# Kernel optimization log

Hardware: AMD Instinct MI355X
Metric: run time of the kernel (lower is better)

Reference implementation:

```python
import jax, jax.numpy as jnp
import numpy as np

B, Lq, Lkv = 4, 1024, 4096
Cq, Ckv, E, NH = 512, 512, 512, 8
HD = E // NH


def setup_inputs() -> dict:
    key = jax.random.key(0)
    ks = jax.random.split(key, 8)
    s = 0.02
    return {
        "Xq": jax.random.normal(ks[0], (B, Lq, Cq), dtype=jnp.float32),
        "Xkv": jax.random.normal(ks[1], (B, Lkv, Ckv), dtype=jnp.float32),
        "mask": jax.random.randint(ks[2], (B, Lq, 1), 0, 2, dtype=jnp.int32),
        "Wq": jax.random.normal(ks[3], (Cq, E), dtype=jnp.float32) * s,
        "bq": jnp.zeros((E,), dtype=jnp.float32),
        "Wkv": jax.random.normal(ks[4], (Ckv, 2 * E), dtype=jnp.float32) * s,
        "bkv": jnp.zeros((2 * E,), dtype=jnp.float32),
        "Wp": jax.random.normal(ks[5], (E, E), dtype=jnp.float32) * s,
        "bp": jnp.zeros((E,), dtype=jnp.float32),
        "attn_pos": jax.random.normal(ks[6], (1, NH, Lq, Lkv), dtype=jnp.float32) * s,
    }


def reference(Xq, Xkv, mask, Wq, bq, Wkv, bkv, Wp, bp, attn_pos):
    scale = HD ** -0.5
    # projections
    Q = (Xq @ Wq + bq).reshape(B, Lq, NH, HD).transpose(0, 2, 1, 3) * scale  # [B,NH,Lq,HD]
    KV = (Xkv @ Wkv + bkv).reshape(B, Lkv, 2, NH, HD)
    K = KV[:, :, 0].transpose(0, 2, 1, 3)  # [B,NH,Lkv,HD]
    V = KV[:, :, 1].transpose(0, 2, 1, 3)
    # scores + learned positional bias
    attn = jnp.einsum('bhqd,bhkd->bhqk', Q, K) + attn_pos  # [B,NH,Lq,Lkv]
    # dummy-column masked softmax (mask: [B,Lq,1], 1=keep row)
    m = mask.astype(attn.dtype)[:, None]           # [B,1,Lq,1]
    attn = attn + (1.0 - m) * (-100.0)             # suppress masked query rows
    dummy = jnp.broadcast_to(jnp.where(m == 0, 100.0, -100.0), (B, NH, Lq, 1))
    attn = jax.nn.softmax(jnp.concatenate([attn, dummy], axis=-1), axis=-1)[..., :Lkv]
    # weighted sum + output projection (dropout = identity in eval)
    out = jnp.einsum('bhqk,bhkd->bhqd', attn, V)
    out = out.transpose(0, 2, 1, 3).reshape(B, Lq, E)
    return out @ Wp + bp
```

## Files before the change

### kernel.cpp

```cpp
#include <hip/hip_runtime.h>

typedef unsigned short u16;
typedef __attribute__((ext_vector_type(8))) short bf16x8;
typedef __attribute__((ext_vector_type(4))) float f32x4;
typedef __attribute__((ext_vector_type(2))) unsigned u32x2;
typedef __attribute__((ext_vector_type(4))) unsigned u32x4;

__device__ __forceinline__ u16 f2bf(float x) {
    union { float f; unsigned u; } v; v.f = x;
    unsigned r = v.u + 0x7FFF + ((v.u >> 16) & 1);
    return (u16)(r >> 16);
}

__device__ __forceinline__ unsigned cvt_pk_bf16(float lo, float hi) {
    unsigned r;
    asm("v_cvt_pk_bf16_f32 %0, %1, %2" : "=v"(r) : "v"(lo), "v"(hi));
    return r;
}

__device__ __forceinline__ bf16x8 pk8(const f32x4& s0, const f32x4& s1) {
    union { u32x4 u; bf16x8 v; } x;
    x.u[0] = cvt_pk_bf16(s0[0], s0[1]);
    x.u[1] = cvt_pk_bf16(s0[2], s0[3]);
    x.u[2] = cvt_pk_bf16(s1[0], s1[1]);
    x.u[3] = cvt_pk_bf16(s1[2], s1[3]);
    return x.v;
}

__device__ __forceinline__ void gl_lds16(const u16* g, u16* l) {
    __builtin_amdgcn_global_load_lds((const __attribute__((address_space(1))) void*)g,
                                     (__attribute__((address_space(3))) void*)l, 16, 0, 0);
}

__global__ __launch_bounds__(256) void conv_bf16_2(const float* __restrict__ Xq,
                                                   const float* __restrict__ Xkv,
                                                   u16* __restrict__ oq,
                                                   u16* __restrict__ okv) {
    int bid = blockIdx.x;
    const float* in;
    u16* out;
    size_t i;
    if (bid < 1024) {
        in = Xq; out = oq;
        i = ((size_t)bid * 256 + threadIdx.x) * 8;
    } else {
        in = Xkv; out = okv;
        i = ((size_t)(bid - 1024) * 256 + threadIdx.x) * 8;
    }
    const float4* p = (const float4*)(in + i);
    float4 a = p[0], b = p[1];
    u32x4 w = {cvt_pk_bf16(a.x, a.y), cvt_pk_bf16(a.z, a.w),
               cvt_pk_bf16(b.x, b.y), cvt_pk_bf16(b.z, b.w)};
    *(u32x4*)(out + i) = w;
}

__global__ __launch_bounds__(256) void transpose_w3(const float* __restrict__ Wq,
                                                    const float* __restrict__ Wkv,
                                                    const float* __restrict__ Wp,
                                                    u16* __restrict__ WqT,
                                                    u16* __restrict__ WkvT,
                                                    u16* __restrict__ WpT) {
    __shared__ float tile[64][65];
    int bid = blockIdx.x;
    const float* in;
    u16* out;
    int R = 512, C, bx, by;
    if (bid < 64) {
        in = Wq; out = WqT; C = 512; bx = bid & 7; by = bid >> 3;
    } else if (bid < 192) {
        bid -= 64;
        in = Wkv; out = WkvT; C = 1024; bx = bid & 15; by = bid >> 4;
    } else {
        bid -= 192;
        in = Wp; out = WpT; C = 512; bx = bid & 7; by = bid >> 3;
    }
    int r0 = by * 64, c0 = bx * 64;
    int tid = threadIdx.x;
#pragma unroll
    for (int j = 0; j < 16; ++j) {
        int e = tid + j * 256;
        int row = e >> 6, col = e & 63;
        tile[row][col] = in[(size_t)(r0 + row) * C + c0 + col];
    }
    __syncthreads();
#pragma unroll
    for (int j = 0; j < 16; ++j) {
        int e = tid + j * 256;
        int row = e >> 6, col = e & 63;
        out[(size_t)(c0 + row) * R + r0 + col] = f2bf(tile[col][row]);
    }
}

template <int MODE>
__global__ __launch_bounds__(256) void gemm_kernel(const u16* __restrict__ A,
                                                   const u16* __restrict__ Bt,
                                                   const float* __restrict__ bias,
                                                   void* __restrict__ Cout,
                                                   void* __restrict__ Cout2,
                                                   int M, int N, int K) {
    __shared__ u16 Al[128][64];
    __shared__ u16 Bl[128][64];
    int tid = threadIdx.x;
    int lane = tid & 63, wid = tid >> 6;
    int wr = wid >> 1, wc = wid & 1;
    int l15 = lane & 15, g = lane >> 4;
    int bm = blockIdx.y, bn = blockIdx.x;
    int ldr = lane >> 3, ldc = (lane & 7) << 3;

    f32x4 acc[4][4];
#pragma unroll
    for (int m = 0; m < 4; ++m)
#pragma unroll
        for (int n = 0; n < 4; ++n)
#pragma unroll
            for (int j = 0; j < 4; ++j) acc[m][n][j] = 0.f;

    int nK = K >> 6;
    for (int kt = 0; kt < nK; ++kt) {
        __syncthreads();
#pragma unroll
        for (int i = 0; i < 4; ++i) {
            int c = wid * 4 + i;
            int row = c * 8 + ldr;
            gl_lds16(A + (size_t)(bm * 128 + row) * K + kt * 64 + ldc, &Al[0][0] + c * 512);
            gl_lds16(Bt + (size_t)(bn * 128 + row) * K + kt * 64 + ldc, &Bl[0][0] + c * 512);
        }
        __syncthreads();

#pragma unroll
        for (int kk = 0; kk < 2; ++kk) {
            bf16x8 af[4], bfr[4];
#pragma unroll
            for (int m = 0; m < 4; ++m)
                af[m] = *(const bf16x8*)&Al[wr * 64 + m * 16 + l15][kk * 32 + g * 8];
#pragma unroll
            for (int n = 0; n < 4; ++n)
                bfr[n] = *(const bf16x8*)&Bl[wc * 64 + n * 16 + l15][kk * 32 + g * 8];
#pragma unroll
            for (int m = 0; m < 4; ++m)
#pragma unroll
                for (int n = 0; n < 4; ++n)
                    acc[m][n] =
                        __builtin_amdgcn_mfma_f32_16x16x32_bf16(af[m], bfr[n], acc[m][n], 0, 0, 0);
        }
    }

#pragma unroll
    for (int m = 0; m < 4; ++m)
#pragma unroll
        for (int n = 0; n < 4; ++n)
#pragma unroll
            for (int j = 0; j < 4; ++j) {
                int row = bm * 128 + wr * 64 + m * 16 + g * 4 + j;
                int col = bn * 128 + wc * 64 + n * 16 + l15;
                float v = acc[m][n][j] + bias[col];
                if (MODE == 1) {
                    int b = row >> 12, kv = row & 4095;
                    if (col < 512) {
                        int h = col >> 6, d = col & 63;
                        ((u16*)Cout)[(((size_t)((b * 8 + h) * 4096 + kv)) << 6) + d] = f2bf(v);
                    } else {
                        int c2 = col - 512;
                        int h = c2 >> 6, d = c2 & 63;
                        int p = j | ((m & 1) << 2) | (g << 3);
                        int dkv = (kv & ~31) | p;
                        ((u16*)Cout2)[((size_t)(b * 8 + h) * 64 + d) * 4096 + dkv] = f2bf(v);
                    }
                } else {
                    ((float*)Cout)[(size_t)row * N + col] = v;
                }
            }
}

template <int MODE>
__global__ __launch_bounds__(256) void gemm_n64(const u16* __restrict__ A,
                                                const u16* __restrict__ Bt,
                                                const float* __restrict__ bias,
                                                void* __restrict__ Cout,
                                                int M, int N, int K) {
    __shared__ u16 Al[128][64];
    __shared__ u16 Bl[64][64];
    int tid = threadIdx.x;
    int lane = tid & 63, wid = tid >> 6;
    int wr = wid >> 1, wc = wid & 1;
    int l15 = lane & 15, g = lane >> 4;
    int bm = blockIdx.y, bn = blockIdx.x;
    int ldr = lane >> 3, ldc = (lane & 7) << 3;

    f32x4 acc[4][2];
#pragma unroll
    for (int m = 0; m < 4; ++m)
#pragma unroll
        for (int n = 0; n < 2; ++n)
#pragma unroll
            for (int j = 0; j < 4; ++j) acc[m][n][j] = 0.f;

    int nK = K >> 6;
    for (int kt = 0; kt < nK; ++kt) {
        __syncthreads();
#pragma unroll
        for (int i = 0; i < 6; ++i) {
            int c = wid * 6 + i;
            if (c < 16) {
                int row = c * 8 + ldr;
                gl_lds16(A + (size_t)(bm * 128 + row) * K + kt * 64 + ldc, &Al[0][0] + c * 512);
            } else {
                int cb = c - 16;
                int row = cb * 8 + ldr;
                gl_lds16(Bt + (size_t)(bn * 64 + row) * K + kt * 64 + ldc, &Bl[0][0] + cb * 512);
            }
        }
        __syncthreads();

#pragma unroll
        for (int kk = 0; kk < 2; ++kk) {
            bf16x8 af[4], bfr[2];
#pragma unroll
            for (int m = 0; m < 4; ++m)
                af[m] = *(const bf16x8*)&Al[wr * 64 + m * 16 + l15][kk * 32 + g * 8];
#pragma unroll
            for (int n = 0; n < 2; ++n)
                bfr[n] = *(const bf16x8*)&Bl[wc * 32 + n * 16 + l15][kk * 32 + g * 8];
#pragma unroll
            for (int m = 0; m < 4; ++m)
#pragma unroll
                for (int n = 0; n < 2; ++n)
                    acc[m][n] =
                        __builtin_amdgcn_mfma_f32_16x16x32_bf16(af[m], bfr[n], acc[m][n], 0, 0, 0);
        }
    }

#pragma unroll
    for (int m = 0; m < 4; ++m)
#pragma unroll
        for (int n = 0; n < 2; ++n)
#pragma unroll
            for (int j = 0; j < 4; ++j) {
                int row = bm * 128 + wr * 64 + m * 16 + g * 4 + j;
                int col = bn * 64 + wc * 32 + n * 16 + l15;
                float v = acc[m][n][j] + bias[col];
                if (MODE == 0) {
                    int b = row >> 10, q = row & 1023, h = col >> 6, d = col & 63;
                    ((u16*)Cout)[(((size_t)((b * 8 + h) * 1024 + q)) << 6) + d] =
                        f2bf(v * 0.18033688011112042f);
                } else {
                    ((float*)Cout)[(size_t)row * N + col] = v;
                }
            }
}

__global__ __launch_bounds__(256, 2) void attn_kernel(const u16* __restrict__ Qb,
                                                      const u16* __restrict__ Kb,
                                                      const u16* __restrict__ Vt,
                                                      const float* __restrict__ pos,
                                                      float* __restrict__ Opart,
                                                      float* __restrict__ Lp) {
    __shared__ u16 Klds[2][4][2048];
    __shared__ u16 Vlds[2][4][2048];

    int idx = blockIdx.x;
    int h = idx & 7;
    int rest = idx >> 3;
    int qt = rest & 15, sp = rest >> 4;
    int q0 = qt * 64;
    int kvbase = sp * 1024;
    int tid = threadIdx.x, lane = tid & 63, wid = tid >> 6;
    int l15 = lane & 15, g = lane >> 4;

    bf16x8 aq[4][2];
#pragma unroll
    for (int b = 0; b < 4; ++b) {
        const u16* qp =
            Qb + (((size_t)((b * 8 + h) * 1024 + q0 + wid * 16 + l15)) << 6) + g * 8;
        aq[b][0] = *(const bf16x8*)(qp);
        aq[b][1] = *(const bf16x8*)(qp + 32);
    }

    f32x4 o[4][4];
    f32x4 lacc[4];
#pragma unroll
    for (int b = 0; b < 4; ++b) {
#pragma unroll
        for (int j = 0; j < 4; ++j) lacc[b][j] = 0.f;
#pragma unroll
        for (int n = 0; n < 4; ++n)
#pragma unroll
            for (int j = 0; j < 4; ++j) o[b][n][j] = 0.f;
    }

    const u16* Kg = Kb + ((size_t)(wid * 8 + h)) * 4096 * 64;
    const u16* Vg = Vt + ((size_t)(wid * 8 + h)) * 4096 * 64;
    int lr = lane >> 3;
    int lcs = ((lane & 7) ^ lr) << 3;
    int vhalf = (lane >> 2) & 1;
    int vslot = (lane & 3) ^ (lr & 3);

    const float* posq =
        pos + (size_t)h * 1024 * 4096 + (size_t)(q0 + wid * 16 + l15) * 4096 + kvbase;

    const short one_s = (short)0x3F80;
    bf16x8 ones = {one_s, one_s, one_s, one_s, one_s, one_s, one_s, one_s};
    int sw = (l15 & 7) << 4;

    auto STAGE = [&](int buf, int t) {
        int kv0 = kvbase + t * 32;
#pragma unroll
        for (int c = 0; c < 4; ++c) {
            gl_lds16(Kg + (size_t)(kv0 + c * 8 + lr) * 64 + lcs, &Klds[buf][wid][c * 512]);
            gl_lds16(Vg + (size_t)(2 * (c * 8 + lr) + vhalf) * 4096 + kv0 + vslot * 8,
                     &Vlds[buf][wid][c * 512]);
        }
    };

    STAGE(0, 0);
    f32x4 zr[2];
#pragma unroll
    for (int n = 0; n < 2; ++n) {
        zr[n] = *(const f32x4*)(posq + n * 16 + g * 4);
#pragma unroll
        for (int j = 0; j < 4; ++j) zr[n][j] *= 1.44269504f;
    }

    for (int kt = 0; kt < 32; ++kt) {
        int cur = kt & 1;
        __syncthreads();

        f32x4 zn0, zn1;
        if (kt < 31) {
            zn0 = *(const f32x4*)(posq + (kt + 1) * 32 + g * 4);
            zn1 = *(const f32x4*)(posq + (kt + 1) * 32 + 16 + g * 4);
            __builtin_amdgcn_sched_barrier(0);
            STAGE(cur ^ 1, kt + 1);
        }

#pragma unroll
        for (int b = 0; b < 4; ++b) {
            const char* KbL = (const char*)&Klds[cur][b][0];
            const char* VbL = (const char*)&Vlds[cur][b][0];

            f32x4 s[2];
            __builtin_amdgcn_s_setprio(1);
#pragma unroll
            for (int n = 0; n < 2; ++n) {
                bf16x8 kb0 = *(const bf16x8*)(KbL + (n * 16 + l15) * 128 + ((g * 16) ^ sw));
                bf16x8 kb1 = *(const bf16x8*)(KbL + (n * 16 + l15) * 128 + ((64 + g * 16) ^ sw));
                f32x4 t = __builtin_amdgcn_mfma_f32_16x16x32_bf16(kb0, aq[b][0], zr[n], 0, 0, 0);
                s[n] = __builtin_amdgcn_mfma_f32_16x16x32_bf16(kb1, aq[b][1], t, 0, 0, 0);
            }
            __builtin_amdgcn_s_setprio(0);

#pragma unroll
            for (int n = 0; n < 2; ++n)
#pragma unroll
                for (int j = 0; j < 4; ++j) s[n][j] = __builtin_exp2f(s[n][j]);

            bf16x8 pa = pk8(s[0], s[1]);

            __builtin_amdgcn_s_setprio(1);
#pragma unroll
            for (int n = 0; n < 4; ++n) {
                int vd = n * 16 + l15;
                int vr = vd >> 1;
                int vbyte = (vr << 7) + ((vd & 1) << 6) + (((g ^ (vr & 3)) & 3) << 4);
                bf16x8 vb = *(const bf16x8*)(VbL + vbyte);
                o[b][n] = __builtin_amdgcn_mfma_f32_16x16x32_bf16(pa, vb, o[b][n], 0, 0, 0);
            }
            lacc[b] = __builtin_amdgcn_mfma_f32_16x16x32_bf16(pa, ones, lacc[b], 0, 0, 0);
            __builtin_amdgcn_s_setprio(0);
        }

        if (kt < 31) {
#pragma unroll
            for (int j = 0; j < 4; ++j) {
                zr[0][j] = zn0[j] * 1.44269504f;
                zr[1][j] = zn1[j] * 1.44269504f;
            }
        }
    }

#pragma unroll
    for (int b = 0; b < 4; ++b) {
        int obase = (sp * 32 + b * 8 + h) * 1024;
#pragma unroll
        for (int j = 0; j < 4; ++j) {
            int row = q0 + wid * 16 + g * 4 + j;
#pragma unroll
            for (int n = 0; n < 4; ++n)
                __builtin_nontemporal_store(o[b][n][j],
                                            &Opart[((size_t)(obase + row)) * 64 + n * 16 + l15]);
            if (l15 == 0) __builtin_nontemporal_store(lacc[b][j], &Lp[obase + row]);
        }
    }
}

__global__ __launch_bounds__(256) void attn_combine(const float* __restrict__ Opart,
                                                    const float* __restrict__ Lp,
                                                    const int* __restrict__ mask,
                                                    u16* __restrict__ AO) {
    int tid = threadIdx.x;
    int d = tid & 63;
    int r = blockIdx.x * 4 + (tid >> 6);
    int bh = r >> 10, q = r & 1023;
    int b = bh >> 3, h = bh & 7;

    float L = 0.f, val = 0.f;
#pragma unroll
    for (int s2 = 0; s2 < 4; ++s2) {
        size_t rr = (size_t)(s2 * 32 + bh) * 1024 + q;
        L += Lp[rr];
        val += Opart[rr * 64 + d];
    }
    float res = mask[b * 1024 + q] ? (val / L) : 0.f;
    AO[((size_t)(b * 1024 + q)) * 512 + h * 64 + d] = f2bf(res);
}

extern "C" void kernel_launch(void* const* d_in, const int* in_sizes, int n_in,
                              void* d_out, int out_size, void* d_ws, size_t ws_size,
                              hipStream_t stream) {
    const float* Xq = (const float*)d_in[0];
    const float* Xkv = (const float*)d_in[1];
    const int* mask = (const int*)d_in[2];
    const float* Wq = (const float*)d_in[3];
    const float* bq = (const float*)d_in[4];
    const float* Wkv = (const float*)d_in[5];
    const float* bkv = (const float*)d_in[6];
    const float* Wp = (const float*)d_in[7];
    const float* bp = (const float*)d_in[8];
    const float* pos = (const float*)d_in[9];
    float* out = (float*)d_out;

    char* ws = (char*)d_ws;
    u16* WqT = (u16*)(ws);
    u16* WkvT = (u16*)(ws + 524288);
    u16* WpT = (u16*)(ws + 1572864);
    u16* Qb = (u16*)(ws + 2097152);
    u16* Kb = (u16*)(ws + 6291456);
    u16* Vt = (u16*)(ws + 23068672);
    u16* AO = (u16*)(ws + 39845888);
    float* Opart = (float*)(ws + 44040192);
    u16* Xkvb = (u16*)(ws + 44040192);
    u16* Xqb = (u16*)(ws + 60817408);
    float* Lp = (float*)(ws + 111149056);

    conv_bf16_2<<<dim3(5120), 256, 0, stream>>>(Xq, Xkv, Xqb, Xkvb);
    transpose_w3<<<dim3(256), 256, 0, stream>>>(Wq, Wkv, Wp, WqT, WkvT, WpT);
    gemm_n64<0><<<dim3(8, 32), 256, 0, stream>>>(Xqb, WqT, bq, Qb, 4096, 512, 512);
    gemm_kernel<1><<<dim3(8, 128), 256, 0, stream>>>(Xkvb, WkvT, bkv, Kb, Vt, 16384, 1024, 512);
    attn_kernel<<<dim3(512), 256, 0, stream>>>(Qb, Kb, Vt, pos, Opart, Lp);
    attn_combine<<<dim3(8192), 256, 0, stream>>>(Opart, Lp, mask, AO);
    gemm_n64<2><<<dim3(8, 32), 256, 0, stream>>>(AO, WpT, bp, out, 4096, 512, 512);
}
```

Before: 190.8 us.

## Drop LDS double buffering in attention kernel to raise occupancy to four blocks

Removes the ping-pong K/V LDS buffers and the register prefetch of the next positional-bias tile. Each iteration now loads its tile synchronously between two barriers, and launch bounds ask for four resident blocks per CU instead of two. The aim is to hide memory latency through higher occupancy rather than software pipelining, which halves LDS use and frees prefetch registers. The cost is exposed load latency inside each block, an extra barrier per iteration, and possible register spilling under the tighter launch bound.

```diff
diff --git a/kernel.cpp b/kernel.cpp
--- a/kernel.cpp
+++ b/kernel.cpp
@@ -249,14 +249,14 @@
             }
 }
 
-__global__ __launch_bounds__(256, 2) void attn_kernel(const u16* __restrict__ Qb,
+__global__ __launch_bounds__(256, 4) void attn_kernel(const u16* __restrict__ Qb,
                                                       const u16* __restrict__ Kb,
                                                       const u16* __restrict__ Vt,
                                                       const float* __restrict__ pos,
                                                       float* __restrict__ Opart,
                                                       float* __restrict__ Lp) {
-    __shared__ u16 Klds[2][4][2048];
-    __shared__ u16 Vlds[2][4][2048];
+    __shared__ u16 Klds[4][2048];
+    __shared__ u16 Vlds[4][2048];
 
     int idx = blockIdx.x;
     int h = idx & 7;
@@ -290,6 +290,8 @@
 
     const u16* Kg = Kb + ((size_t)(wid * 8 + h)) * 4096 * 64;
     const u16* Vg = Vt + ((size_t)(wid * 8 + h)) * 4096 * 64;
+    u16* KldsW = &Klds[wid][0];
+    u16* VldsW = &Vlds[wid][0];
     int lr = lane >> 3;
     int lcs = ((lane & 7) ^ lr) << 3;
     int vhalf = (lane >> 2) & 1;
@@ -302,41 +304,29 @@
     bf16x8 ones = {one_s, one_s, one_s, one_s, one_s, one_s, one_s, one_s};
     int sw = (l15 & 7) << 4;
 
-    auto STAGE = [&](int buf, int t) {
-        int kv0 = kvbase + t * 32;
-#pragma unroll
-        for (int c = 0; c < 4; ++c) {
-            gl_lds16(Kg + (size_t)(kv0 + c * 8 + lr) * 64 + lcs, &Klds[buf][wid][c * 512]);
+    f32x4 zr[2];
+    for (int kt = 0; kt < 32; ++kt) {
+        int kv0 = kvbase + kt * 32;
+        __syncthreads();
+#pragma unroll
+        for (int c = 0; c < 4; ++c)
+            gl_lds16(Kg + (size_t)(kv0 + c * 8 + lr) * 64 + lcs, KldsW + c * 512);
+#pragma unroll
+        for (int c = 0; c < 4; ++c)
             gl_lds16(Vg + (size_t)(2 * (c * 8 + lr) + vhalf) * 4096 + kv0 + vslot * 8,
-                     &Vlds[buf][wid][c * 512]);
-        }
-    };
-
-    STAGE(0, 0);
-    f32x4 zr[2];
-#pragma unroll
-    for (int n = 0; n < 2; ++n) {
-        zr[n] = *(const f32x4*)(posq + n * 16 + g * 4);
-#pragma unroll
-        for (int j = 0; j < 4; ++j) zr[n][j] *= 1.44269504f;
-    }
-
-    for (int kt = 0; kt < 32; ++kt) {
-        int cur = kt & 1;
-        __syncthreads();
-
-        f32x4 zn0, zn1;
-        if (kt < 31) {
-            zn0 = *(const f32x4*)(posq + (kt + 1) * 32 + g * 4);
-            zn1 = *(const f32x4*)(posq + (kt + 1) * 32 + 16 + g * 4);
-            __builtin_amdgcn_sched_barrier(0);
-            STAGE(cur ^ 1, kt + 1);
-        }
+                     VldsW + c * 512);
+#pragma unroll
+        for (int n = 0; n < 2; ++n) {
+            zr[n] = *(const f32x4*)(posq + kt * 32 + n * 16 + g * 4);
+#pragma unroll
+            for (int j = 0; j < 4; ++j) zr[n][j] *= 1.44269504f;
+        }
+        __syncthreads();
 
 #pragma unroll
         for (int b = 0; b < 4; ++b) {
-            const char* KbL = (const char*)&Klds[cur][b][0];
-            const char* VbL = (const char*)&Vlds[cur][b][0];
+            const char* KbL = (const char*)&Klds[b][0];
+            const char* VbL = (const char*)&Vlds[b][0];
 
             f32x4 s[2];
             __builtin_amdgcn_s_setprio(1);
@@ -367,14 +357,6 @@
             }
             lacc[b] = __builtin_amdgcn_mfma_f32_16x16x32_bf16(pa, ones, lacc[b], 0, 0, 0);
             __builtin_amdgcn_s_setprio(0);
-        }
-
-        if (kt < 31) {
-#pragma unroll
-            for (int j = 0; j < 4; ++j) {
-                zr[0][j] = zn0[j] * 1.44269504f;
-                zr[1][j] = zn1[j] * 1.44269504f;
-            }
         }
     }
 
```

Measured after the change: 256.3 us. 34.3% more time.
